# Kernel optimization log

Measured on AMD Instinct MI355X. Metric: run time of the kernel, lower is better.

## Reference

```python
import jax, jax.numpy as jnp
import numpy as np

B, IN, H = 4096, 1024, 1024


def setup_inputs() -> dict:
    key = jax.random.key(0)
    ks = jax.random.split(key, 16)
    s_in = 1.0 / np.sqrt(IN)
    s_h = 1.0 / np.sqrt(H)
    d = {
        "x_t": jax.random.normal(ks[0], (B, IN), jnp.float32),
        "h_prev": jax.random.normal(ks[1], (B, H), jnp.float32),
        "c_prev": jax.random.normal(ks[2], (B, H), jnp.float32),
    }
    # input->hidden weights (with bias), stored torch-style as (out, in)
    for i, name in enumerate(["ii", "if", "ig", "io"]):
        d[f"W_{name}"] = jax.random.uniform(ks[3 + i], (H, IN), jnp.float32, -s_in, s_in)
        d[f"b_{name}"] = jax.random.uniform(ks[7 + i], (H,), jnp.float32, -s_in, s_in)
    # hidden->hidden weights (no bias)
    for i, name in enumerate(["hi", "hf", "hg", "ho"]):
        d[f"W_{name}"] = jax.random.uniform(ks[11 + i], (H, H), jnp.float32, -s_h, s_h)
    return d


def reference(x_t, h_prev, c_prev,
              W_ii, b_ii, W_if, b_if, W_ig, b_ig, W_io, b_io,
              W_hi, W_hf, W_hg, W_ho):
    # Fuse the 8 small GEMMs into 2 concatenated GEMMs (same math).
    Wx = jnp.concatenate([W_ii, W_if, W_ig, W_io], axis=0)   # (4H, IN)
    Wh = jnp.concatenate([W_hi, W_hf, W_hg, W_ho], axis=0)   # (4H, H)
    b = jnp.concatenate([b_ii, b_if, b_ig, b_io], axis=0)    # (4H,)
    gates = x_t @ Wx.T + h_prev @ Wh.T + b                    # (B, 4H)
    zi, zf, zg, zo = jnp.split(gates, 4, axis=1)
    i_t = jax.nn.sigmoid(zi)
    f_t = jax.nn.sigmoid(zf)
    g_t = jnp.tanh(zg)
    o_t = jax.nn.sigmoid(zo)
    c_t = f_t * c_prev + i_t * g_t
    h_t = o_t * jnp.tanh(c_t)
    return (h_t, c_t, (i_t, f_t, g_t, o_t))
```

## Files before the change

### kernel.cpp

```cpp
#include <hip/hip_runtime.h>
#include <hip/hip_bf16.h>

#define B_DIM 4096
#define K_TOT 2048
#define H_DIM 1024

typedef short bf16x8 __attribute__((ext_vector_type(8)));
typedef float f32x4 __attribute__((ext_vector_type(4)));
typedef unsigned short u16x8 __attribute__((ext_vector_type(8)));

typedef __attribute__((address_space(1))) const unsigned gas_u32;
typedef __attribute__((address_space(3))) unsigned las_u32;

static __device__ __forceinline__ unsigned short f2bf(float f) {
  union { float f; unsigned u; } v; v.f = f;
  unsigned r = v.u + 0x7FFF + ((v.u >> 16) & 1);
  return (unsigned short)(r >> 16);
}

__global__ void pack_all(const float* __restrict__ x, const float* __restrict__ hp,
                         const float* __restrict__ W0, const float* __restrict__ W1,
                         const float* __restrict__ W2, const float* __restrict__ W3,
                         const float* __restrict__ W4, const float* __restrict__ W5,
                         const float* __restrict__ W6, const float* __restrict__ W7,
                         u16x8* __restrict__ A, u16x8* __restrict__ Wc) {
  int blk = blockIdx.x;
  const float* src;
  u16x8* dst;
  int t;
  if (blk < 4096) {
    t = blk * blockDim.x + threadIdx.x;
    int idx = t << 3;
    int b = idx >> 11;
    int k = idx & 2047;
    src = (k < 1024) ? (x + b * 1024 + k) : (hp + b * 1024 + (k - 1024));
    dst = A + t;
  } else {
    t = (blk - 4096) * blockDim.x + threadIdx.x;
    int idx = t << 3;
    int n = idx >> 11;
    int k = idx & 2047;
    int gate = n >> 10;
    int j = n & 1023;
    int s = (k < 1024) ? gate : gate + 4;
    const float* base =
        (s == 0) ? W0 : (s == 1) ? W1 : (s == 2) ? W2 : (s == 3) ? W3 :
        (s == 4) ? W4 : (s == 5) ? W5 : (s == 6) ? W6 : W7;
    src = base + j * 1024 + (k & 1023);
    dst = Wc + t;
  }
  float4 lo = *(const float4*)src;
  float4 hi = *(const float4*)(src + 4);
  u16x8 v;
  v[0] = f2bf(lo.x); v[1] = f2bf(lo.y); v[2] = f2bf(lo.z); v[3] = f2bf(lo.w);
  v[4] = f2bf(hi.x); v[5] = f2bf(hi.y); v[6] = f2bf(hi.z); v[7] = f2bf(hi.w);
  *dst = v;
}

static __device__ __forceinline__ float sigm(float x) {
  return 1.0f / (1.0f + __expf(-x));
}
static __device__ __forceinline__ float tanh_fast(float x) {
  x = fminf(fmaxf(x, -15.f), 15.f);
  float t = __expf(-2.0f * x);
  return (1.0f - t) / (1.0f + t);
}

__global__ __launch_bounds__(128) void gemm_lstm(
    const unsigned short* __restrict__ A,
    const unsigned short* __restrict__ W,
    const float* __restrict__ cp,
    const float* __restrict__ bii, const float* __restrict__ bif,
    const float* __restrict__ big, const float* __restrict__ bio,
    float* __restrict__ out) {
  __shared__ unsigned short As[64 * 32];
  __shared__ unsigned short Bs[128 * 32];
  const int tid = threadIdx.x;
  const int wave = tid >> 6;
  const int lane = tid & 63;
  const int m0 = blockIdx.y << 6;
  const int j0 = blockIdx.x << 5;
  const int wj16 = wave << 4;

  f32x4 acc[4][4];
#pragma unroll
  for (int mi = 0; mi < 4; ++mi)
#pragma unroll
    for (int ni = 0; ni < 4; ++ni)
      acc[mi][ni] = (f32x4){0.f, 0.f, 0.f, 0.f};

  const int lr = lane >> 2;
  const int ls = lane & 3;
  const int g  = ls ^ ((lr >> 1) & 3);

  const int ca = wave * 2;
  const unsigned short* aptr0 = A + (long)(m0 + ca * 16 + lr) * K_TOT + g * 8;
  const unsigned short* aptr1 = A + (long)(m0 + (ca + 1) * 16 + lr) * K_TOT + g * 8;
  char* lA0 = (char*)As + ca * 1024;
  char* lA1 = lA0 + 1024;

  const int cb = wave * 4;
  const unsigned short* bptr[4];
  char* lB[4];
#pragma unroll
  for (int q = 0; q < 4; ++q) {
    int rr = (cb + q) * 16 + lr;
    bptr[q] = W + (long)((rr >> 5) * 1024 + j0 + (rr & 31)) * K_TOT + g * 8;
    lB[q] = (char*)Bs + (cb + q) * 1024;
  }

  const int fr = lane & 15;
  const int gg = lane >> 4;
  const int sl = (gg ^ ((fr >> 1) & 3)) * 16;

  for (int k0 = 0; k0 < K_TOT; k0 += 32) {
    __builtin_amdgcn_global_load_lds((gas_u32*)(aptr0 + k0), (las_u32*)lA0, 16, 0, 0);
    __builtin_amdgcn_global_load_lds((gas_u32*)(aptr1 + k0), (las_u32*)lA1, 16, 0, 0);
#pragma unroll
    for (int q = 0; q < 4; ++q)
      __builtin_amdgcn_global_load_lds((gas_u32*)(bptr[q] + k0), (las_u32*)lB[q], 16, 0, 0);
    __syncthreads();
    bf16x8 af[4], bfv[4];
#pragma unroll
    for (int i = 0; i < 4; ++i) {
      af[i]  = *(const bf16x8*)((const char*)As + (i * 16 + fr) * 64 + sl);
      bfv[i] = *(const bf16x8*)((const char*)Bs + (i * 32 + wj16 + fr) * 64 + sl);
    }
#pragma unroll
    for (int mi = 0; mi < 4; ++mi)
#pragma unroll
      for (int ni = 0; ni < 4; ++ni)
        acc[mi][ni] = __builtin_amdgcn_mfma_f32_16x16x32_bf16(af[mi], bfv[ni], acc[mi][ni], 0, 0, 0);
    __syncthreads();
  }

  const int ccol = lane & 15;
  const int crow = (lane >> 4) * 4;
  const int j = j0 + wj16 + ccol;
  const float bi = bii[j];
  const float bff = bif[j];
  const float bg = big[j];
  const float bo = bio[j];
  const long BH = (long)B_DIM * H_DIM;
#pragma unroll
  for (int mi = 0; mi < 4; ++mi) {
#pragma unroll
    for (int reg = 0; reg < 4; ++reg) {
      const int row = m0 + mi * 16 + crow + reg;
      const long p = (long)row * H_DIM + j;
      const float cvp = cp[p];
      const float iv = sigm(acc[mi][0][reg] + bi);
      const float fv = sigm(acc[mi][1][reg] + bff);
      const float gv = tanh_fast(acc[mi][2][reg] + bg);
      const float ov = sigm(acc[mi][3][reg] + bo);
      const float cv = fv * cvp + iv * gv;
      const float hv = ov * tanh_fast(cv);
      out[p]          = hv;
      out[BH + p]     = cv;
      out[2 * BH + p] = iv;
      out[3 * BH + p] = fv;
      out[4 * BH + p] = gv;
      out[5 * BH + p] = ov;
    }
  }
}

extern "C" void kernel_launch(void* const* d_in, const int* in_sizes, int n_in,
                              void* d_out, int out_size, void* d_ws, size_t ws_size,
                              hipStream_t stream) {
  const float* x    = (const float*)d_in[0];
  const float* h    = (const float*)d_in[1];
  const float* c    = (const float*)d_in[2];
  const float* W_ii = (const float*)d_in[3];
  const float* b_ii = (const float*)d_in[4];
  const float* W_if = (const float*)d_in[5];
  const float* b_if = (const float*)d_in[6];
  const float* W_ig = (const float*)d_in[7];
  const float* b_ig = (const float*)d_in[8];
  const float* W_io = (const float*)d_in[9];
  const float* b_io = (const float*)d_in[10];
  const float* W_hi = (const float*)d_in[11];
  const float* W_hf = (const float*)d_in[12];
  const float* W_hg = (const float*)d_in[13];
  const float* W_ho = (const float*)d_in[14];

  unsigned short* Abf = (unsigned short*)d_ws;
  unsigned short* Wbf = (unsigned short*)((char*)d_ws + (size_t)16 * 1024 * 1024);

  pack_all<<<8192, 256, 0, stream>>>(x, h, W_ii, W_if, W_ig, W_io,
                                     W_hi, W_hf, W_hg, W_ho,
                                     (u16x8*)Abf, (u16x8*)Wbf);
  dim3 grid(H_DIM / 32, B_DIM / 64);
  gemm_lstm<<<grid, 128, 0, stream>>>(Abf, Wbf, c, b_ii, b_if, b_ig, b_io,
                                      (float*)d_out);
}
```

Baseline: 316.6 us.

## Drop LDS staging and load MFMA fragments directly from global memory

Removes the shared-memory tiles, global_load_lds staging and both barriers per K step. Each wave now reads its A and W fragments straight from global memory into registers. The block grows to 256 threads covering 64 hidden columns, with four waves each owning 16 columns. All four waves in a block reload the same A rows and no tile is reused through LDS, so cache traffic rises, while barrier stalls go away.

```diff
diff --git a/kernel.cpp b/kernel.cpp
--- a/kernel.cpp
+++ b/kernel.cpp
@@ -8,9 +8,6 @@
 typedef short bf16x8 __attribute__((ext_vector_type(8)));
 typedef float f32x4 __attribute__((ext_vector_type(4)));
 typedef unsigned short u16x8 __attribute__((ext_vector_type(8)));
-
-typedef __attribute__((address_space(1))) const unsigned gas_u32;
-typedef __attribute__((address_space(3))) unsigned las_u32;
 
 static __device__ __forceinline__ unsigned short f2bf(float f) {
   union { float f; unsigned u; } v; v.f = f;
@@ -66,21 +63,22 @@
   return (1.0f - t) / (1.0f + t);
 }
 
-__global__ __launch_bounds__(128) void gemm_lstm(
+__global__ __launch_bounds__(256) void gemm_lstm(
     const unsigned short* __restrict__ A,
     const unsigned short* __restrict__ W,
     const float* __restrict__ cp,
     const float* __restrict__ bii, const float* __restrict__ bif,
     const float* __restrict__ big, const float* __restrict__ bio,
     float* __restrict__ out) {
-  __shared__ unsigned short As[64 * 32];
-  __shared__ unsigned short Bs[128 * 32];
-  const int tid = threadIdx.x;
-  const int wave = tid >> 6;
-  const int lane = tid & 63;
+  const int wave = threadIdx.x >> 6;
+  const int lane = threadIdx.x & 63;
   const int m0 = blockIdx.y << 6;
-  const int j0 = blockIdx.x << 5;
-  const int wj16 = wave << 4;
+  const int j0 = (blockIdx.x << 6) + (wave << 4);
+  const int fr = lane & 15;
+  const int gg = lane >> 4;
+
+  const unsigned short* aB = A + (long)(m0 + fr) * K_TOT + gg * 8;
+  const unsigned short* bB = W + (long)(j0 + fr) * K_TOT + gg * 8;
 
   f32x4 acc[4][4];
 #pragma unroll
@@ -89,54 +87,24 @@
     for (int ni = 0; ni < 4; ++ni)
       acc[mi][ni] = (f32x4){0.f, 0.f, 0.f, 0.f};
 
-  const int lr = lane >> 2;
-  const int ls = lane & 3;
-  const int g  = ls ^ ((lr >> 1) & 3);
-
-  const int ca = wave * 2;
-  const unsigned short* aptr0 = A + (long)(m0 + ca * 16 + lr) * K_TOT + g * 8;
-  const unsigned short* aptr1 = A + (long)(m0 + (ca + 1) * 16 + lr) * K_TOT + g * 8;
-  char* lA0 = (char*)As + ca * 1024;
-  char* lA1 = lA0 + 1024;
-
-  const int cb = wave * 4;
-  const unsigned short* bptr[4];
-  char* lB[4];
-#pragma unroll
-  for (int q = 0; q < 4; ++q) {
-    int rr = (cb + q) * 16 + lr;
-    bptr[q] = W + (long)((rr >> 5) * 1024 + j0 + (rr & 31)) * K_TOT + g * 8;
-    lB[q] = (char*)Bs + (cb + q) * 1024;
-  }
-
-  const int fr = lane & 15;
-  const int gg = lane >> 4;
-  const int sl = (gg ^ ((fr >> 1) & 3)) * 16;
-
+#pragma unroll 2
   for (int k0 = 0; k0 < K_TOT; k0 += 32) {
-    __builtin_amdgcn_global_load_lds((gas_u32*)(aptr0 + k0), (las_u32*)lA0, 16, 0, 0);
-    __builtin_amdgcn_global_load_lds((gas_u32*)(aptr1 + k0), (las_u32*)lA1, 16, 0, 0);
-#pragma unroll
-    for (int q = 0; q < 4; ++q)
-      __builtin_amdgcn_global_load_lds((gas_u32*)(bptr[q] + k0), (las_u32*)lB[q], 16, 0, 0);
-    __syncthreads();
     bf16x8 af[4], bfv[4];
 #pragma unroll
     for (int i = 0; i < 4; ++i) {
-      af[i]  = *(const bf16x8*)((const char*)As + (i * 16 + fr) * 64 + sl);
-      bfv[i] = *(const bf16x8*)((const char*)Bs + (i * 32 + wj16 + fr) * 64 + sl);
+      af[i]  = *(const bf16x8*)(aB + (long)(i * 16) * K_TOT + k0);
+      bfv[i] = *(const bf16x8*)(bB + (long)(i * 1024) * K_TOT + k0);
     }
 #pragma unroll
     for (int mi = 0; mi < 4; ++mi)
 #pragma unroll
       for (int ni = 0; ni < 4; ++ni)
         acc[mi][ni] = __builtin_amdgcn_mfma_f32_16x16x32_bf16(af[mi], bfv[ni], acc[mi][ni], 0, 0, 0);
-    __syncthreads();
   }
 
   const int ccol = lane & 15;
   const int crow = (lane >> 4) * 4;
-  const int j = j0 + wj16 + ccol;
+  const int j = j0 + ccol;
   const float bi = bii[j];
   const float bff = bif[j];
   const float bg = big[j];
@@ -190,7 +158,7 @@
   pack_all<<<8192, 256, 0, stream>>>(x, h, W_ii, W_if, W_ig, W_io,
                                      W_hi, W_hf, W_hg, W_ho,
                                      (u16x8*)Abf, (u16x8*)Wbf);
-  dim3 grid(H_DIM / 32, B_DIM / 64);
-  gemm_lstm<<<grid, 128, 0, stream>>>(Abf, Wbf, c, b_ii, b_if, b_ig, b_io,
+  dim3 grid(H_DIM / 64, B_DIM / 64);
+  gemm_lstm<<<grid, 256, 0, stream>>>(Abf, Wbf, c, b_ii, b_if, b_ig, b_io,
                                       (float*)d_out);
 }
```

Result: slower. 423.1 us (+33.6%).
